# Performance work log

Measured on AMD Instinct MI355X. Metric: run time of the kernel, lower is better.

The kernel has to match this reference:

```python
import jax, jax.numpy as jnp
import numpy as np

N_NODES = 100000


def _add_self_loops(edge_index, n):
    loop = jnp.arange(n, dtype=edge_index.dtype)
    src = jnp.concatenate([edge_index[0], loop])
    dst = jnp.concatenate([edge_index[1], loop])
    return src, dst


def _gcn_conv(x, src, dst, dinv_src, dinv_dst, W, b, n):
    # linear transform first (PyG GCNConv), then normalized scatter-add
    h = x @ W                                   # [N, out]
    msg = h[src] * (dinv_src * dinv_dst)[:, None]  # [E+N, out] gather
    out = jax.ops.segment_sum(msg, dst, num_segments=n)
    return out + b


def reference(x, edge_index, W0, b0, W1, b1, Wf, bf):
    n = N_NODES
    src, dst = _add_self_loops(edge_index, n)
    ones = jnp.ones(src.shape[0], dtype=x.dtype)
    deg = jax.ops.segment_sum(ones, dst, num_segments=n)
    dinv = jnp.where(deg > 0, jax.lax.rsqrt(jnp.maximum(deg, 1.0)), 0.0)
    dinv_src = dinv[src]
    dinv_dst = dinv[dst]

    h = jax.nn.relu(_gcn_conv(x, src, dst, dinv_src, dinv_dst, W0, b0, n))
    h = jax.nn.relu(_gcn_conv(h, src, dst, dinv_src, dinv_dst, W1, b1, n))
    return h @ Wf + bf


def setup_inputs() -> dict:
    key = jax.random.key(0)
    ks = jax.random.split(key, 8)
    n, e, f, h = N_NODES, 1600000, 32, 32
    return {
        "x": jax.random.normal(ks[0], (n, f), dtype=jnp.float32),
        "edge_index": jax.random.randint(ks[1], (2, e), 0, n, dtype=jnp.int64),
        "W0": jax.random.normal(ks[2], (f, h), dtype=jnp.float32) / np.sqrt(f),
        "b0": jnp.zeros((h,), dtype=jnp.float32),
        "W1": jax.random.normal(ks[3], (h, h), dtype=jnp.float32) / np.sqrt(h),
        "b1": jnp.zeros((h,), dtype=jnp.float32),
        "Wf": jax.random.normal(ks[4], (h, h), dtype=jnp.float32) / np.sqrt(h),
        "bf": jnp.zeros((h,), dtype=jnp.float32),
    }
```

## Files before the change

### kernel.cpp

```cpp
#include <hip/hip_runtime.h>
#include <hip/hip_fp16.h>


#define GNN_F 32
#define NBKT 391
#define BCAP 5120
#define CHUNK 8192

__global__ __launch_bounds__(256) void k_fused1(
    const float* __restrict__ x, const float* __restrict__ W0,
    __half* __restrict__ t,
    const int* __restrict__ src, const int* __restrict__ dst,
    int* bcnt, int* __restrict__ queue,
    int n, int e, int gemmBlocks) {
    __shared__ float Wl[32 * 32];
    __shared__ int hist4[4 * NBKT], curs[NBKT], base[NBKT];
    int tid = threadIdx.x;

    if (blockIdx.x < gemmBlocks) {
        if (blockIdx.x == 0 && tid < 4) {
            uint4 z = make_uint4(0u, 0u, 0u, 0u);
            ((uint4*)(t + (size_t)n * 32))[tid] = z;
        }
        ((float4*)Wl)[tid] = ((const float4*)W0)[tid];
        __syncthreads();
        int r = blockIdx.x * 256 + tid;
        if (r >= n) return;
        float xr[32];
        const float4* in4 = (const float4*)(x + (size_t)r * 32);
#pragma unroll
        for (int j = 0; j < 8; ++j) {
            float4 v = in4[j];
            xr[4 * j + 0] = v.x; xr[4 * j + 1] = v.y;
            xr[4 * j + 2] = v.z; xr[4 * j + 3] = v.w;
        }
        float acc[32];
#pragma unroll
        for (int c = 0; c < 32; ++c) acc[c] = 0.0f;
#pragma unroll
        for (int k = 0; k < 32; ++k) {
            float xv = xr[k];
#pragma unroll
            for (int c = 0; c < 32; ++c) acc[c] = fmaf(xv, Wl[k * 32 + c], acc[c]);
        }
        uint4* tp = (uint4*)(t + (size_t)r * 32);
#pragma unroll
        for (int j = 0; j < 4; ++j) {
            __half2 h0 = __floats2half2_rn(acc[8 * j + 0], acc[8 * j + 1]);
            __half2 h1 = __floats2half2_rn(acc[8 * j + 2], acc[8 * j + 3]);
            __half2 h2 = __floats2half2_rn(acc[8 * j + 4], acc[8 * j + 5]);
            __half2 h3 = __floats2half2_rn(acc[8 * j + 6], acc[8 * j + 7]);
            uint4 o;
            o.x = *(unsigned*)&h0; o.y = *(unsigned*)&h1;
            o.z = *(unsigned*)&h2; o.w = *(unsigned*)&h3;
            tp[j] = o;
        }
    } else {
        int c0 = (blockIdx.x - gemmBlocks) * CHUNK;
        int g0 = c0 >> 2;
        int n4 = e >> 2;
        int cpy = (tid & 3) * NBKT;
        for (int i = tid; i < 4 * NBKT; i += 256) hist4[i] = 0;
        __syncthreads();
#pragma unroll
        for (int p = 0; p < CHUNK / 1024; ++p) {
            int g = g0 + p * 256 + tid;
            if (g < n4) {
                int4 d = ((const int4*)dst)[g];
                atomicAdd(&hist4[cpy + (((unsigned)d.x) >> 8)], 1);
                atomicAdd(&hist4[cpy + (((unsigned)d.y) >> 8)], 1);
                atomicAdd(&hist4[cpy + (((unsigned)d.z) >> 8)], 1);
                atomicAdd(&hist4[cpy + (((unsigned)d.w) >> 8)], 1);
            }
        }
        int tail0 = e & ~3;
        if (tail0 >= c0 && tail0 < c0 + CHUNK && tid < (e & 3))
            atomicAdd(&hist4[cpy + (((unsigned)dst[tail0 + tid]) >> 8)], 1);
        __syncthreads();
        for (int b = tid; b < NBKT; b += 256) {
            int h = hist4[b] + hist4[NBKT + b] + hist4[2 * NBKT + b] + hist4[3 * NBKT + b];
            base[b] = h ? atomicAdd(&bcnt[b], h) : 0;
            curs[b] = 0;
        }
        __syncthreads();
#pragma unroll
        for (int p = 0; p < CHUNK / 1024; ++p) {
            int g = g0 + p * 256 + tid;
            if (g < n4) {
                int4 d = ((const int4*)dst)[g];
                int4 sv = ((const int4*)src)[g];
                int b, l, slot;
                b = ((unsigned)d.x) >> 8; l = atomicAdd(&curs[b], 1); slot = base[b] + l;
                if (slot < BCAP) queue[(size_t)b * BCAP + slot] = (sv.x << 8) | (d.x & 255);
                b = ((unsigned)d.y) >> 8; l = atomicAdd(&curs[b], 1); slot = base[b] + l;
                if (slot < BCAP) queue[(size_t)b * BCAP + slot] = (sv.y << 8) | (d.y & 255);
                b = ((unsigned)d.z) >> 8; l = atomicAdd(&curs[b], 1); slot = base[b] + l;
                if (slot < BCAP) queue[(size_t)b * BCAP + slot] = (sv.z << 8) | (d.z & 255);
                b = ((unsigned)d.w) >> 8; l = atomicAdd(&curs[b], 1); slot = base[b] + l;
                if (slot < BCAP) queue[(size_t)b * BCAP + slot] = (sv.w << 8) | (d.w & 255);
            }
        }
        if (tail0 >= c0 && tail0 < c0 + CHUNK && tid < (e & 3)) {
            int j = tail0 + tid;
            int d = dst[j];
            int b = ((unsigned)d) >> 8;
            int l = atomicAdd(&curs[b], 1);
            int slot = base[b] + l;
            if (slot < BCAP) queue[(size_t)b * BCAP + slot] = (src[j] << 8) | (d & 255);
        }
    }
}

__global__ __launch_bounds__(256) void k_build(
    const int* __restrict__ bcnt, const int* __restrict__ queue,
    int* __restrict__ csr, int* __restrict__ rs, float* __restrict__ dinv,
    __half* __restrict__ t, int n) {
    __shared__ int red[256];
    __shared__ int hist2[2 * 256], sh[256], cur[256];
    __shared__ float dsh[256];
    int b = blockIdx.x;
    int tid = threadIdx.x;

    int part = 0;
    for (int i = tid; i < b; i += 256) {
        int v = bcnt[i];
        part += (v > BCAP ? BCAP : v);
    }
    red[tid] = part;
    hist2[tid] = 0;
    hist2[256 + tid] = 0;
    __syncthreads();
#pragma unroll
    for (int off = 128; off > 0; off >>= 1) {
        if (tid < off) red[tid] += red[tid + off];
        __syncthreads();
    }
    int bbase = red[0];

    int len = bcnt[b];
    if (len > BCAP) len = BCAP;
    const int* q = queue + (size_t)b * BCAP;

    int cpy = (tid & 1) << 8;
    for (int i = tid; i < len; i += 256) atomicAdd(&hist2[cpy + (q[i] & 255)], 1);
    __syncthreads();
    int c = hist2[tid] + hist2[256 + tid];
    sh[tid] = c;
    __syncthreads();
    for (int off = 1; off < 256; off <<= 1) {
        int xv = (tid >= off) ? sh[tid - off] : 0;
        __syncthreads();
        sh[tid] += xv;
        __syncthreads();
    }
    int myStart = bbase + sh[tid] - c;
    int node = (b << 8) + tid;
    float dv = rsqrtf((float)(c + 1));
    if (node < n) {
        rs[node] = myStart;
        dinv[node] = dv;
    }
    if (b == (int)gridDim.x - 1 && tid == 255) rs[n] = myStart + c;
    dsh[tid] = dv;
    cur[tid] = myStart;
    __syncthreads();
    for (int i = tid; i < len; i += 256) {
        int qq = q[i];
        int p = atomicAdd(&cur[qq & 255], 1);
        csr[p] = ((unsigned)qq) >> 8;
    }
    int rows = n - (b << 8);
    if (rows > 256) rows = 256;
    if (rows < 0) rows = 0;
    uint4* t4 = (uint4*)(t + ((size_t)b << 8) * 32);
    for (int i = tid; i < rows * 4; i += 256) {
        float d = dsh[i >> 2];
        uint4 v = t4[i];
        __half2 h0 = *(__half2*)&v.x, h1 = *(__half2*)&v.y;
        __half2 h2 = *(__half2*)&v.z, h3 = *(__half2*)&v.w;
        float2 f0 = __half22float2(h0), f1 = __half22float2(h1);
        float2 f2 = __half22float2(h2), f3 = __half22float2(h3);
        h0 = __floats2half2_rn(f0.x * d, f0.y * d);
        h1 = __floats2half2_rn(f1.x * d, f1.y * d);
        h2 = __floats2half2_rn(f2.x * d, f2.y * d);
        h3 = __floats2half2_rn(f3.x * d, f3.y * d);
        v.x = *(unsigned*)&h0; v.y = *(unsigned*)&h1;
        v.z = *(unsigned*)&h2; v.w = *(unsigned*)&h3;
        t4[i] = v;
    }
}

#define LOAD4(u, A, B)                                         \
    {                                                          \
        uint2 raw = ((const uint2*)(t + (size_t)(u) * 32))[j]; \
        __half2 p0 = *(__half2*)&raw.x;                        \
        __half2 p1 = *(__half2*)&raw.y;                        \
        A = __half22float2(p0);                                \
        B = __half22float2(p1);                                \
    }

#define GIDX(k_, uvar)                       \
    {                                        \
        int ik = e + (k_);                   \
        bool ok = ik < e1;                   \
        uvar = csr[ok ? ik : last];          \
        uvar = ok ? uvar : n;                \
    }

#define GATHER_BODY()                                                          \
    int idx = blockIdx.x * 256 + threadIdx.x;                                  \
    int tid = threadIdx.x;                                                     \
    int row = idx >> 3;                                                        \
    bool live = row < n;                                                       \
    if (!live) row = n - 1;                                                    \
    int j = tid & 7;                                                           \
    int e0 = rs[row];                                                          \
    int e1 = rs[row + 1];                                                      \
    ((float4*)Wl)[tid] = ((const float4*)W)[tid];                              \
    __syncthreads();                                                           \
    int last = e1 - 1;                                                         \
    float2 sa, sb;                                                             \
    LOAD4(row, sa, sb);                                                        \
    float d = dinv[row];                                                       \
    float ax = 0.f, ay = 0.f, az = 0.f, aw = 0.f;                              \
    int e = e0;                                                                \
    int rem = e1 - e0;                                                         \
    int u0, u1, u2, u3, u4, u5, u6, u7;                                        \
    if (rem > 0) {                                                             \
        u0 = csr[e];                                                           \
        GIDX(1, u1) GIDX(2, u2) GIDX(3, u3)                                    \
        GIDX(4, u4) GIDX(5, u5) GIDX(6, u6) GIDX(7, u7)                        \
    }                                                                          \
    while (rem > 0) {                                                          \
        float2 a0, b0v, a1, b1v, a2, b2v, a3, b3v;                             \
        float2 a4, b4v, a5, b5v, a6, b6v, a7, b7v;                             \
        LOAD4(u0, a0, b0v); LOAD4(u1, a1, b1v);                                \
        LOAD4(u2, a2, b2v); LOAD4(u3, a3, b3v);                                \
        LOAD4(u4, a4, b4v); LOAD4(u5, a5, b5v);                                \
        LOAD4(u6, a6, b6v); LOAD4(u7, a7, b7v);                                \
        e += 8; rem -= 8;                                                      \
        if (rem > 0) {                                                         \
            u0 = csr[e];                                                       \
            GIDX(1, u1) GIDX(2, u2) GIDX(3, u3)                                \
            GIDX(4, u4) GIDX(5, u5) GIDX(6, u6) GIDX(7, u7)                    \
        }                                                                      \
        ax += ((a0.x + a1.x) + (a2.x + a3.x)) + ((a4.x + a5.x) + (a6.x + a7.x));\
        ay += ((a0.y + a1.y) + (a2.y + a3.y)) + ((a4.y + a5.y) + (a6.y + a7.y));\
        az += ((b0v.x + b1v.x) + (b2v.x + b3v.x)) + ((b4v.x + b5v.x) + (b6v.x + b7v.x));\
        aw += ((b0v.y + b1v.y) + (b2v.y + b3v.y)) + ((b4v.y + b5v.y) + (b6v.y + b7v.y));\
    }                                                                          \
    float4 pb4 = ((const float4*)preb)[j];                                     \
    float4 u4v;                                                                \
    u4v.x = fmaxf(d * (ax + sa.x) + pb4.x, 0.0f);                              \
    u4v.y = fmaxf(d * (ay + sa.y) + pb4.y, 0.0f);                              \
    u4v.z = fmaxf(d * (az + sb.x) + pb4.z, 0.0f);                              \
    u4v.w = fmaxf(d * (aw + sb.y) + pb4.w, 0.0f);                              \
    int wv = tid >> 6;                                                         \
    int g = (tid >> 3) & 7;                                                    \
    float* urow = ur + wv * 320 + g * 40;                                      \
    *(float4*)(urow + 4 * j) = u4v;                                            \
       \
                \
    asm volatile("s_waitcnt lgkmcnt(0)" ::: "memory");

__global__ __launch_bounds__(256) void k_gather_gemm(
    const int* __restrict__ rs, const int* __restrict__ csr,
    const float* __restrict__ dinv, const __half* __restrict__ t,
    const float* __restrict__ W, const float* __restrict__ preb,
    __half* __restrict__ t_out, int n) {
    __shared__ float Wl[32 * 32];
    __shared__ float ur[4 * 320];
    if (blockIdx.x == 0 && threadIdx.x < 4) {
        uint4 z = make_uint4(0u, 0u, 0u, 0u);
        ((uint4*)(t_out + (size_t)n * 32))[threadIdx.x] = z;
    }
    GATHER_BODY()
    float4 o = make_float4(0.f, 0.f, 0.f, 0.f);
#pragma unroll
    for (int k = 0; k < 32; ++k) {
        float uk = urow[k];
        float4 wv4 = ((const float4*)(Wl + k * 32))[j];
        o.x = fmaf(uk, wv4.x, o.x);
        o.y = fmaf(uk, wv4.y, o.y);
        o.z = fmaf(uk, wv4.z, o.z);
        o.w = fmaf(uk, wv4.w, o.w);
    }
    o.x *= d; o.y *= d; o.z *= d; o.w *= d;
    if (live) {
        __half2 h0 = __floats2half2_rn(o.x, o.y);
        __half2 h1 = __floats2half2_rn(o.z, o.w);
        uint2 pk;
        pk.x = *(unsigned*)&h0; pk.y = *(unsigned*)&h1;
        ((uint2*)(t_out + (size_t)row * 32))[j] = pk;
    }
}

__global__ __launch_bounds__(256) void k_gather_out(
    const int* __restrict__ rs, const int* __restrict__ csr,
    const float* __restrict__ dinv, const __half* __restrict__ t,
    const float* __restrict__ W, const float* __restrict__ preb,
    const float* __restrict__ postb, float* __restrict__ out, int n) {
    __shared__ float Wl[32 * 32];
    __shared__ float ur[4 * 320];
    GATHER_BODY()
    float4 o = ((const float4*)postb)[j];
#pragma unroll
    for (int k = 0; k < 32; ++k) {
        float uk = urow[k];
        float4 wv4 = ((const float4*)(Wl + k * 32))[j];
        o.x = fmaf(uk, wv4.x, o.x);
        o.y = fmaf(uk, wv4.y, o.y);
        o.z = fmaf(uk, wv4.z, o.z);
        o.w = fmaf(uk, wv4.w, o.w);
    }
    if (live) ((float4*)(out + (size_t)row * 32))[j] = o;
}

extern "C" void kernel_launch(void* const* d_in, const int* in_sizes, int n_in,
                              void* d_out, int out_size, void* d_ws, size_t ws_size,
                              hipStream_t stream) {
    const float* x  = (const float*)d_in[0];
    const int*   ei = (const int*)d_in[1];
    const float* W0 = (const float*)d_in[2];
    const float* b0 = (const float*)d_in[3];
    const float* W1 = (const float*)d_in[4];
    const float* b1 = (const float*)d_in[5];
    const float* Wf = (const float*)d_in[6];
    const float* bf = (const float*)d_in[7];
    float* out = (float*)d_out;

    const int N = in_sizes[0] / GNN_F;
    const int E = in_sizes[1] / 2;
    const int* srcI = ei;
    const int* dstI = ei + E;

    const int gN = (N + 255) / 256;
    const int gG = (N * 8 + 255) / 256;
    const int nChunk = (E + CHUNK - 1) / CHUNK;

    char* ws = (char*)d_ws;
    size_t off = 0;
    auto alloc = [&](size_t bytes) {
        void* p = ws + off;
        off += (bytes + 127) & ~(size_t)127;
        return p;
    };
    int*    bcnt  = (int*)alloc((size_t)NBKT * 4);
    int*    rs    = (int*)alloc((size_t)(N + 1) * 4);
    float*  dinv  = (float*)alloc((size_t)N * 4);
    int*    queue = (int*)alloc((size_t)NBKT * BCAP * 4);
    int*    csr   = (int*)alloc((size_t)E * 4);
    __half* t_a   = (__half*)alloc((size_t)(N + 1) * GNN_F * 2);
    __half* t_b   = (__half*)alloc((size_t)(N + 1) * GNN_F * 2);
    (void)ws_size;

    hipMemsetAsync(bcnt, 0, (size_t)NBKT * 4, stream);

    k_fused1<<<gN + nChunk, 256, 0, stream>>>(x, W0, t_a, srcI, dstI, bcnt,
                                              queue, N, E, gN);
    k_build<<<NBKT, 256, 0, stream>>>(bcnt, queue, csr, rs, dinv, t_a, N);

    k_gather_gemm<<<gG, 256, 0, stream>>>(rs, csr, dinv, t_a, W1, b0, t_b, N);

    k_gather_out<<<gG, 256, 0, stream>>>(rs, csr, dinv, t_b, Wf, b1, bf, out, N);
}
```

Before: 162.6 us.

## Software-pipeline neighbor feature loads and use shuffles for per-row GEMM

The gather loop now issues the next batch of eight neighbor feature loads before reducing the current batch, a software pipeline that keeps more memory requests in flight per thread. The small per-row 32x32 GEMM also drops its shared-memory staging buffer: each thread's activation values are broadcast within the 8-lane row group via __shfl instead of being written to and read from LDS. This saves LDS traffic and shared memory but raises register pressure from the doubled load buffers, which could lower occupancy.

```diff
diff --git a/kernel.cpp b/kernel.cpp
--- a/kernel.cpp
+++ b/kernel.cpp
@@ -225,43 +225,63 @@
     float ax = 0.f, ay = 0.f, az = 0.f, aw = 0.f;                              \
     int e = e0;                                                                \
     int rem = e1 - e0;                                                         \
-    int u0, u1, u2, u3, u4, u5, u6, u7;                                        \
-    if (rem > 0) {                                                             \
+    float2 a0, b0v, a1, b1v, a2, b2v, a3, b3v;                                 \
+    float2 a4, b4v, a5, b5v, a6, b6v, a7, b7v;                                 \
+    if (rem > 0) {             \
+        int u0, u1, u2, u3, u4, u5, u6, u7;                                    \
         u0 = csr[e];                                                           \
         GIDX(1, u1) GIDX(2, u2) GIDX(3, u3)                                    \
         GIDX(4, u4) GIDX(5, u5) GIDX(6, u6) GIDX(7, u7)                        \
-    }                                                                          \
-    while (rem > 0) {                                                          \
-        float2 a0, b0v, a1, b1v, a2, b2v, a3, b3v;                             \
-        float2 a4, b4v, a5, b5v, a6, b6v, a7, b7v;                             \
         LOAD4(u0, a0, b0v); LOAD4(u1, a1, b1v);                                \
         LOAD4(u2, a2, b2v); LOAD4(u3, a3, b3v);                                \
         LOAD4(u4, a4, b4v); LOAD4(u5, a5, b5v);                                \
         LOAD4(u6, a6, b6v); LOAD4(u7, a7, b7v);                                \
+    }                                                                          \
+    while (rem > 0) {                                                          \
         e += 8; rem -= 8;                                                      \
-        if (rem > 0) {                                                         \
-            u0 = csr[e];                                                       \
-            GIDX(1, u1) GIDX(2, u2) GIDX(3, u3)                                \
-            GIDX(4, u4) GIDX(5, u5) GIDX(6, u6) GIDX(7, u7)                    \
+        float2 na0, nb0, na1, nb1, na2, nb2, na3, nb3;                         \
+        float2 na4, nb4, na5, nb5, na6, nb6, na7, nb7;                         \
+        if (rem > 0) {     \
+            int v0, v1, v2, v3, v4, v5, v6, v7;                                \
+            v0 = csr[e];                                                       \
+            GIDX(1, v1) GIDX(2, v2) GIDX(3, v3)                                \
+            GIDX(4, v4) GIDX(5, v5) GIDX(6, v6) GIDX(7, v7)                    \
+            LOAD4(v0, na0, nb0); LOAD4(v1, na1, nb1);                          \
+            LOAD4(v2, na2, nb2); LOAD4(v3, na3, nb3);                          \
+            LOAD4(v4, na4, nb4); LOAD4(v5, na5, nb5);                          \
+            LOAD4(v6, na6, nb6); LOAD4(v7, na7, nb7);                          \
         }                                                                      \
         ax += ((a0.x + a1.x) + (a2.x + a3.x)) + ((a4.x + a5.x) + (a6.x + a7.x));\
         ay += ((a0.y + a1.y) + (a2.y + a3.y)) + ((a4.y + a5.y) + (a6.y + a7.y));\
         az += ((b0v.x + b1v.x) + (b2v.x + b3v.x)) + ((b4v.x + b5v.x) + (b6v.x + b7v.x));\
         aw += ((b0v.y + b1v.y) + (b2v.y + b3v.y)) + ((b4v.y + b5v.y) + (b6v.y + b7v.y));\
+        if (rem > 0) {                                                         \
+            a0 = na0; b0v = nb0; a1 = na1; b1v = nb1;                          \
+            a2 = na2; b2v = nb2; a3 = na3; b3v = nb3;                          \
+            a4 = na4; b4v = nb4; a5 = na5; b5v = nb5;                          \
+            a6 = na6; b6v = nb6; a7 = na7; b7v = nb7;                          \
+        }                                                                      \
     }                                                                          \
     float4 pb4 = ((const float4*)preb)[j];                                     \
     float4 u4v;                                                                \
     u4v.x = fmaxf(d * (ax + sa.x) + pb4.x, 0.0f);                              \
     u4v.y = fmaxf(d * (ay + sa.y) + pb4.y, 0.0f);                              \
     u4v.z = fmaxf(d * (az + sb.x) + pb4.z, 0.0f);                              \
-    u4v.w = fmaxf(d * (aw + sb.y) + pb4.w, 0.0f);                              \
-    int wv = tid >> 6;                                                         \
-    int g = (tid >> 3) & 7;                                                    \
-    float* urow = ur + wv * 320 + g * 40;                                      \
-    *(float4*)(urow + 4 * j) = u4v;                                            \
-       \
-                \
-    asm volatile("s_waitcnt lgkmcnt(0)" ::: "memory");
+    u4v.w = fmaxf(d * (aw + sb.y) + pb4.w, 0.0f);
+
+#define GEMM_FMA(o_)                                                           \
+    _Pragma("unroll")                                                          \
+    for (int k = 0; k < 32; ++k) {                                             \
+        float comp = ((k & 3) == 0) ? u4v.x                                    \
+                   : ((k & 3) == 1) ? u4v.y                                    \
+                   : ((k & 3) == 2) ? u4v.z : u4v.w;                           \
+        float uk = __shfl(comp, k >> 2, 8);                                    \
+        float4 wv4 = ((const float4*)(Wl + k * 32))[j];                        \
+        o_.x = fmaf(uk, wv4.x, o_.x);                                          \
+        o_.y = fmaf(uk, wv4.y, o_.y);                                          \
+        o_.z = fmaf(uk, wv4.z, o_.z);                                          \
+        o_.w = fmaf(uk, wv4.w, o_.w);                                          \
+    }
 
 __global__ __launch_bounds__(256) void k_gather_gemm(
     const int* __restrict__ rs, const int* __restrict__ csr,
@@ -269,22 +289,13 @@
     const float* __restrict__ W, const float* __restrict__ preb,
     __half* __restrict__ t_out, int n) {
     __shared__ float Wl[32 * 32];
-    __shared__ float ur[4 * 320];
     if (blockIdx.x == 0 && threadIdx.x < 4) {
         uint4 z = make_uint4(0u, 0u, 0u, 0u);
         ((uint4*)(t_out + (size_t)n * 32))[threadIdx.x] = z;
     }
     GATHER_BODY()
     float4 o = make_float4(0.f, 0.f, 0.f, 0.f);
-#pragma unroll
-    for (int k = 0; k < 32; ++k) {
-        float uk = urow[k];
-        float4 wv4 = ((const float4*)(Wl + k * 32))[j];
-        o.x = fmaf(uk, wv4.x, o.x);
-        o.y = fmaf(uk, wv4.y, o.y);
-        o.z = fmaf(uk, wv4.z, o.z);
-        o.w = fmaf(uk, wv4.w, o.w);
-    }
+    GEMM_FMA(o)
     o.x *= d; o.y *= d; o.z *= d; o.w *= d;
     if (live) {
         __half2 h0 = __floats2half2_rn(o.x, o.y);
@@ -301,18 +312,9 @@
     const float* __restrict__ W, const float* __restrict__ preb,
     const float* __restrict__ postb, float* __restrict__ out, int n) {
     __shared__ float Wl[32 * 32];
-    __shared__ float ur[4 * 320];
     GATHER_BODY()
     float4 o = ((const float4*)postb)[j];
-#pragma unroll
-    for (int k = 0; k < 32; ++k) {
-        float uk = urow[k];
-        float4 wv4 = ((const float4*)(Wl + k * 32))[j];
-        o.x = fmaf(uk, wv4.x, o.x);
-        o.y = fmaf(uk, wv4.y, o.y);
-        o.z = fmaf(uk, wv4.z, o.z);
-        o.w = fmaf(uk, wv4.w, o.w);
-    }
+    GEMM_FMA(o)
     if (live) ((float4*)(out + (size_t)row * 32))[j] = o;
 }
 
```

Measured after the change: 178.1 us. 9.5% more time.

## Build CSR via global per-node degree atomics and scatter instead of bucket queue

Applied to the files above, without the earlier changes.

Replaces the two-level bucketed queue CSR build with a per-node global degree count (global atomics in the histogram pass), a prefix-scan in k_build, and a separate k_scatter kernel that places each source into the CSR using global atomic cursors. This removes the intermediate queue buffer, its write and re-read, and the BCAP overflow truncation. In exchange it adds 1.6M global atomics for degree counting and another 1.6M for scattering, with random-address CSR writes and an extra kernel launch. Within-row neighbor order becomes nondeterministic.

```diff
diff --git a/kernel.cpp b/kernel.cpp
--- a/kernel.cpp
+++ b/kernel.cpp
@@ -4,17 +4,16 @@
 
 #define GNN_F 32
 #define NBKT 391
-#define BCAP 5120
 #define CHUNK 8192
 
 __global__ __launch_bounds__(256) void k_fused1(
     const float* __restrict__ x, const float* __restrict__ W0,
     __half* __restrict__ t,
-    const int* __restrict__ src, const int* __restrict__ dst,
-    int* bcnt, int* __restrict__ queue,
+    const int* __restrict__ dst,
+    int* __restrict__ bcnt, int* __restrict__ deg,
     int n, int e, int gemmBlocks) {
     __shared__ float Wl[32 * 32];
-    __shared__ int hist4[4 * NBKT], curs[NBKT], base[NBKT];
+    __shared__ int hist4[4 * NBKT];
     int tid = threadIdx.x;
 
     if (blockIdx.x < gemmBlocks) {
@@ -71,64 +70,39 @@
                 atomicAdd(&hist4[cpy + (((unsigned)d.y) >> 8)], 1);
                 atomicAdd(&hist4[cpy + (((unsigned)d.z) >> 8)], 1);
                 atomicAdd(&hist4[cpy + (((unsigned)d.w) >> 8)], 1);
+                atomicAdd(&deg[d.x], 1);
+                atomicAdd(&deg[d.y], 1);
+                atomicAdd(&deg[d.z], 1);
+                atomicAdd(&deg[d.w], 1);
             }
         }
         int tail0 = e & ~3;
-        if (tail0 >= c0 && tail0 < c0 + CHUNK && tid < (e & 3))
-            atomicAdd(&hist4[cpy + (((unsigned)dst[tail0 + tid]) >> 8)], 1);
+        if (tail0 >= c0 && tail0 < c0 + CHUNK && tid < (e & 3)) {
+            int d = dst[tail0 + tid];
+            atomicAdd(&hist4[cpy + (((unsigned)d) >> 8)], 1);
+            atomicAdd(&deg[d], 1);
+        }
         __syncthreads();
         for (int b = tid; b < NBKT; b += 256) {
             int h = hist4[b] + hist4[NBKT + b] + hist4[2 * NBKT + b] + hist4[3 * NBKT + b];
-            base[b] = h ? atomicAdd(&bcnt[b], h) : 0;
-            curs[b] = 0;
-        }
-        __syncthreads();
-#pragma unroll
-        for (int p = 0; p < CHUNK / 1024; ++p) {
-            int g = g0 + p * 256 + tid;
-            if (g < n4) {
-                int4 d = ((const int4*)dst)[g];
-                int4 sv = ((const int4*)src)[g];
-                int b, l, slot;
-                b = ((unsigned)d.x) >> 8; l = atomicAdd(&curs[b], 1); slot = base[b] + l;
-                if (slot < BCAP) queue[(size_t)b * BCAP + slot] = (sv.x << 8) | (d.x & 255);
-                b = ((unsigned)d.y) >> 8; l = atomicAdd(&curs[b], 1); slot = base[b] + l;
-                if (slot < BCAP) queue[(size_t)b * BCAP + slot] = (sv.y << 8) | (d.y & 255);
-                b = ((unsigned)d.z) >> 8; l = atomicAdd(&curs[b], 1); slot = base[b] + l;
-                if (slot < BCAP) queue[(size_t)b * BCAP + slot] = (sv.z << 8) | (d.z & 255);
-                b = ((unsigned)d.w) >> 8; l = atomicAdd(&curs[b], 1); slot = base[b] + l;
-                if (slot < BCAP) queue[(size_t)b * BCAP + slot] = (sv.w << 8) | (d.w & 255);
-            }
-        }
-        if (tail0 >= c0 && tail0 < c0 + CHUNK && tid < (e & 3)) {
-            int j = tail0 + tid;
-            int d = dst[j];
-            int b = ((unsigned)d) >> 8;
-            int l = atomicAdd(&curs[b], 1);
-            int slot = base[b] + l;
-            if (slot < BCAP) queue[(size_t)b * BCAP + slot] = (src[j] << 8) | (d & 255);
+            if (h) atomicAdd(&bcnt[b], h);
         }
     }
 }
 
 __global__ __launch_bounds__(256) void k_build(
-    const int* __restrict__ bcnt, const int* __restrict__ queue,
-    int* __restrict__ csr, int* __restrict__ rs, float* __restrict__ dinv,
+    const int* __restrict__ bcnt, const int* __restrict__ deg,
+    int* __restrict__ rs, int* __restrict__ cur, float* __restrict__ dinv,
     __half* __restrict__ t, int n) {
     __shared__ int red[256];
-    __shared__ int hist2[2 * 256], sh[256], cur[256];
+    __shared__ int sh[256];
     __shared__ float dsh[256];
     int b = blockIdx.x;
     int tid = threadIdx.x;
 
     int part = 0;
-    for (int i = tid; i < b; i += 256) {
-        int v = bcnt[i];
-        part += (v > BCAP ? BCAP : v);
-    }
+    for (int i = tid; i < b; i += 256) part += bcnt[i];
     red[tid] = part;
-    hist2[tid] = 0;
-    hist2[256 + tid] = 0;
     __syncthreads();
 #pragma unroll
     for (int off = 128; off > 0; off >>= 1) {
@@ -137,14 +111,8 @@
     }
     int bbase = red[0];
 
-    int len = bcnt[b];
-    if (len > BCAP) len = BCAP;
-    const int* q = queue + (size_t)b * BCAP;
-
-    int cpy = (tid & 1) << 8;
-    for (int i = tid; i < len; i += 256) atomicAdd(&hist2[cpy + (q[i] & 255)], 1);
-    __syncthreads();
-    int c = hist2[tid] + hist2[256 + tid];
+    int node = (b << 8) + tid;
+    int c = (node < n) ? deg[node] : 0;
     sh[tid] = c;
     __syncthreads();
     for (int off = 1; off < 256; off <<= 1) {
@@ -154,21 +122,15 @@
         __syncthreads();
     }
     int myStart = bbase + sh[tid] - c;
-    int node = (b << 8) + tid;
     float dv = rsqrtf((float)(c + 1));
     if (node < n) {
         rs[node] = myStart;
         dinv[node] = dv;
+        cur[node] = myStart;
     }
     if (b == (int)gridDim.x - 1 && tid == 255) rs[n] = myStart + c;
     dsh[tid] = dv;
-    cur[tid] = myStart;
     __syncthreads();
-    for (int i = tid; i < len; i += 256) {
-        int qq = q[i];
-        int p = atomicAdd(&cur[qq & 255], 1);
-        csr[p] = ((unsigned)qq) >> 8;
-    }
     int rows = n - (b << 8);
     if (rows > 256) rows = 256;
     if (rows < 0) rows = 0;
@@ -187,6 +149,27 @@
         v.x = *(unsigned*)&h0; v.y = *(unsigned*)&h1;
         v.z = *(unsigned*)&h2; v.w = *(unsigned*)&h3;
         t4[i] = v;
+    }
+}
+
+__global__ __launch_bounds__(256) void k_scatter(
+    const int* __restrict__ src, const int* __restrict__ dst,
+    int* __restrict__ cur, int* __restrict__ csr, int e) {
+    int n4 = e >> 2;
+    int stride = gridDim.x * 256;
+    for (int g = blockIdx.x * 256 + threadIdx.x; g < n4; g += stride) {
+        int4 d = ((const int4*)dst)[g];
+        int4 s = ((const int4*)src)[g];
+        int p0 = atomicAdd(&cur[d.x], 1);
+        int p1 = atomicAdd(&cur[d.y], 1);
+        int p2 = atomicAdd(&cur[d.z], 1);
+        int p3 = atomicAdd(&cur[d.w], 1);
+        csr[p0] = s.x; csr[p1] = s.y; csr[p2] = s.z; csr[p3] = s.w;
+    }
+    if (blockIdx.x == 0 && threadIdx.x < (e & 3)) {
+        int j = (e & ~3) + threadIdx.x;
+        int p = atomicAdd(&cur[dst[j]], 1);
+        csr[p] = src[j];
     }
 }
 
@@ -346,19 +329,21 @@
         return p;
     };
     int*    bcnt  = (int*)alloc((size_t)NBKT * 4);
+    int*    deg   = (int*)alloc((size_t)N * 4);
     int*    rs    = (int*)alloc((size_t)(N + 1) * 4);
+    int*    cur   = (int*)alloc((size_t)N * 4);
     float*  dinv  = (float*)alloc((size_t)N * 4);
-    int*    queue = (int*)alloc((size_t)NBKT * BCAP * 4);
     int*    csr   = (int*)alloc((size_t)E * 4);
     __half* t_a   = (__half*)alloc((size_t)(N + 1) * GNN_F * 2);
     __half* t_b   = (__half*)alloc((size_t)(N + 1) * GNN_F * 2);
     (void)ws_size;
 
-    hipMemsetAsync(bcnt, 0, (size_t)NBKT * 4, stream);
-
-    k_fused1<<<gN + nChunk, 256, 0, stream>>>(x, W0, t_a, srcI, dstI, bcnt,
-                                              queue, N, E, gN);
-    k_build<<<NBKT, 256, 0, stream>>>(bcnt, queue, csr, rs, dinv, t_a, N);
+    hipMemsetAsync(bcnt, 0, (size_t)((char*)rs - (char*)bcnt), stream);
+
+    k_fused1<<<gN + nChunk, 256, 0, stream>>>(x, W0, t_a, dstI, bcnt, deg,
+                                              N, E, gN);
+    k_build<<<NBKT, 256, 0, stream>>>(bcnt, deg, rs, cur, dinv, t_a, N);
+    k_scatter<<<1024, 256, 0, stream>>>(srcI, dstI, cur, csr, E);
 
     k_gather_gemm<<<gG, 256, 0, stream>>>(rs, csr, dinv, t_a, W1, b0, t_b, N);
 
```

Measured after the change: 313.7 us. 92.9% more time.

## Halve bucket width to 128 rows and split feature prescale into its own kernel

Applied to the files above, without the earlier changes.

Bucket granularity drops from 256 to 128 destination rows, doubling the bucket count and halving per-bucket capacity, so k_build launches twice as many blocks, each doing less work. The dinv prescale of the transformed features moves out of k_build into a separate elementwise kernel. The goal is better occupancy and load balance in the CSR build. The cost is an extra kernel launch, larger shared histograms in k_fused1, and a tighter per-bucket capacity that raises the risk of overflow on skewed degree distributions.

```diff
diff --git a/kernel.cpp b/kernel.cpp
--- a/kernel.cpp
+++ b/kernel.cpp
@@ -3,8 +3,9 @@
 
 
 #define GNN_F 32
-#define NBKT 391
-#define BCAP 5120
+#define NBKT 782
+#define BROWS 128
+#define BCAP 2560
 #define CHUNK 8192
 
 __global__ __launch_bounds__(256) void k_fused1(
@@ -67,15 +68,15 @@
             int g = g0 + p * 256 + tid;
             if (g < n4) {
                 int4 d = ((const int4*)dst)[g];
-                atomicAdd(&hist4[cpy + (((unsigned)d.x) >> 8)], 1);
-                atomicAdd(&hist4[cpy + (((unsigned)d.y) >> 8)], 1);
-                atomicAdd(&hist4[cpy + (((unsigned)d.z) >> 8)], 1);
-                atomicAdd(&hist4[cpy + (((unsigned)d.w) >> 8)], 1);
+                atomicAdd(&hist4[cpy + (((unsigned)d.x) >> 7)], 1);
+                atomicAdd(&hist4[cpy + (((unsigned)d.y) >> 7)], 1);
+                atomicAdd(&hist4[cpy + (((unsigned)d.z) >> 7)], 1);
+                atomicAdd(&hist4[cpy + (((unsigned)d.w) >> 7)], 1);
             }
         }
         int tail0 = e & ~3;
         if (tail0 >= c0 && tail0 < c0 + CHUNK && tid < (e & 3))
-            atomicAdd(&hist4[cpy + (((unsigned)dst[tail0 + tid]) >> 8)], 1);
+            atomicAdd(&hist4[cpy + (((unsigned)dst[tail0 + tid]) >> 7)], 1);
         __syncthreads();
         for (int b = tid; b < NBKT; b += 256) {
             int h = hist4[b] + hist4[NBKT + b] + hist4[2 * NBKT + b] + hist4[3 * NBKT + b];
@@ -90,23 +91,23 @@
                 int4 d = ((const int4*)dst)[g];
                 int4 sv = ((const int4*)src)[g];
                 int b, l, slot;
-                b = ((unsigned)d.x) >> 8; l = atomicAdd(&curs[b], 1); slot = base[b] + l;
-                if (slot < BCAP) queue[(size_t)b * BCAP + slot] = (sv.x << 8) | (d.x & 255);
-                b = ((unsigned)d.y) >> 8; l = atomicAdd(&curs[b], 1); slot = base[b] + l;
-                if (slot < BCAP) queue[(size_t)b * BCAP + slot] = (sv.y << 8) | (d.y & 255);
-                b = ((unsigned)d.z) >> 8; l = atomicAdd(&curs[b], 1); slot = base[b] + l;
-                if (slot < BCAP) queue[(size_t)b * BCAP + slot] = (sv.z << 8) | (d.z & 255);
-                b = ((unsigned)d.w) >> 8; l = atomicAdd(&curs[b], 1); slot = base[b] + l;
-                if (slot < BCAP) queue[(size_t)b * BCAP + slot] = (sv.w << 8) | (d.w & 255);
+                b = ((unsigned)d.x) >> 7; l = atomicAdd(&curs[b], 1); slot = base[b] + l;
+                if (slot < BCAP) queue[(size_t)b * BCAP + slot] = (sv.x << 7) | (d.x & 127);
+                b = ((unsigned)d.y) >> 7; l = atomicAdd(&curs[b], 1); slot = base[b] + l;
+                if (slot < BCAP) queue[(size_t)b * BCAP + slot] = (sv.y << 7) | (d.y & 127);
+                b = ((unsigned)d.z) >> 7; l = atomicAdd(&curs[b], 1); slot = base[b] + l;
+                if (slot < BCAP) queue[(size_t)b * BCAP + slot] = (sv.z << 7) | (d.z & 127);
+                b = ((unsigned)d.w) >> 7; l = atomicAdd(&curs[b], 1); slot = base[b] + l;
+                if (slot < BCAP) queue[(size_t)b * BCAP + slot] = (sv.w << 7) | (d.w & 127);
             }
         }
         if (tail0 >= c0 && tail0 < c0 + CHUNK && tid < (e & 3)) {
-            int j = tail0 + tid;
-            int d = dst[j];
-            int b = ((unsigned)d) >> 8;
+            int jg = tail0 + tid;
+            int d = dst[jg];
+            int b = ((unsigned)d) >> 7;
             int l = atomicAdd(&curs[b], 1);
             int slot = base[b] + l;
-            if (slot < BCAP) queue[(size_t)b * BCAP + slot] = (src[j] << 8) | (d & 255);
+            if (slot < BCAP) queue[(size_t)b * BCAP + slot] = (src[jg] << 7) | (d & 127);
         }
     }
 }
@@ -114,10 +115,9 @@
 __global__ __launch_bounds__(256) void k_build(
     const int* __restrict__ bcnt, const int* __restrict__ queue,
     int* __restrict__ csr, int* __restrict__ rs, float* __restrict__ dinv,
-    __half* __restrict__ t, int n) {
+    int n) {
     __shared__ int red[256];
-    __shared__ int hist2[2 * 256], sh[256], cur[256];
-    __shared__ float dsh[256];
+    __shared__ int hist2[2 * BROWS], sh[BROWS], cur[BROWS];
     int b = blockIdx.x;
     int tid = threadIdx.x;
 
@@ -127,8 +127,7 @@
         part += (v > BCAP ? BCAP : v);
     }
     red[tid] = part;
-    hist2[tid] = 0;
-    hist2[256 + tid] = 0;
+    hist2[tid & 255] = 0;
     __syncthreads();
 #pragma unroll
     for (int off = 128; off > 0; off >>= 1) {
@@ -141,53 +140,57 @@
     if (len > BCAP) len = BCAP;
     const int* q = queue + (size_t)b * BCAP;
 
-    int cpy = (tid & 1) << 8;
-    for (int i = tid; i < len; i += 256) atomicAdd(&hist2[cpy + (q[i] & 255)], 1);
+    int cpy = (tid & 1) << 7;
+    for (int i = tid; i < len; i += 256) atomicAdd(&hist2[cpy + (q[i] & 127)], 1);
     __syncthreads();
-    int c = hist2[tid] + hist2[256 + tid];
-    sh[tid] = c;
+    int c = 0;
+    if (tid < BROWS) {
+        c = hist2[tid] + hist2[BROWS + tid];
+        sh[tid] = c;
+    }
     __syncthreads();
-    for (int off = 1; off < 256; off <<= 1) {
-        int xv = (tid >= off) ? sh[tid - off] : 0;
-        __syncthreads();
-        sh[tid] += xv;
-        __syncthreads();
-    }
-    int myStart = bbase + sh[tid] - c;
-    int node = (b << 8) + tid;
-    float dv = rsqrtf((float)(c + 1));
-    if (node < n) {
-        rs[node] = myStart;
-        dinv[node] = dv;
-    }
-    if (b == (int)gridDim.x - 1 && tid == 255) rs[n] = myStart + c;
-    dsh[tid] = dv;
-    cur[tid] = myStart;
+    for (int off = 1; off < BROWS; off <<= 1) {
+        int xv = (tid >= off && tid < BROWS) ? sh[tid - off] : 0;
+        __syncthreads();
+        if (tid < BROWS) sh[tid] += xv;
+        __syncthreads();
+    }
+    if (tid < BROWS) {
+        int myStart = bbase + sh[tid] - c;
+        int node = (b << 7) + tid;
+        if (node < n) {
+            rs[node] = myStart;
+            dinv[node] = rsqrtf((float)(c + 1));
+        }
+        if (b == (int)gridDim.x - 1 && tid == BROWS - 1) rs[n] = myStart + c;
+        cur[tid] = myStart;
+    }
     __syncthreads();
     for (int i = tid; i < len; i += 256) {
         int qq = q[i];
-        int p = atomicAdd(&cur[qq & 255], 1);
-        csr[p] = ((unsigned)qq) >> 8;
-    }
-    int rows = n - (b << 8);
-    if (rows > 256) rows = 256;
-    if (rows < 0) rows = 0;
-    uint4* t4 = (uint4*)(t + ((size_t)b << 8) * 32);
-    for (int i = tid; i < rows * 4; i += 256) {
-        float d = dsh[i >> 2];
-        uint4 v = t4[i];
-        __half2 h0 = *(__half2*)&v.x, h1 = *(__half2*)&v.y;
-        __half2 h2 = *(__half2*)&v.z, h3 = *(__half2*)&v.w;
-        float2 f0 = __half22float2(h0), f1 = __half22float2(h1);
-        float2 f2 = __half22float2(h2), f3 = __half22float2(h3);
-        h0 = __floats2half2_rn(f0.x * d, f0.y * d);
-        h1 = __floats2half2_rn(f1.x * d, f1.y * d);
-        h2 = __floats2half2_rn(f2.x * d, f2.y * d);
-        h3 = __floats2half2_rn(f3.x * d, f3.y * d);
-        v.x = *(unsigned*)&h0; v.y = *(unsigned*)&h1;
-        v.z = *(unsigned*)&h2; v.w = *(unsigned*)&h3;
-        t4[i] = v;
-    }
+        int p = atomicAdd(&cur[qq & 127], 1);
+        csr[p] = ((unsigned)qq) >> 7;
+    }
+}
+
+__global__ __launch_bounds__(256) void k_prescale(
+    const float* __restrict__ dinv, __half* __restrict__ t, int n) {
+    int i = blockIdx.x * 256 + threadIdx.x;
+    if (i >= n * 4) return;
+    float d = dinv[i >> 2];
+    uint4* t4 = (uint4*)t;
+    uint4 v = t4[i];
+    __half2 h0 = *(__half2*)&v.x, h1 = *(__half2*)&v.y;
+    __half2 h2 = *(__half2*)&v.z, h3 = *(__half2*)&v.w;
+    float2 f0 = __half22float2(h0), f1 = __half22float2(h1);
+    float2 f2 = __half22float2(h2), f3 = __half22float2(h3);
+    h0 = __floats2half2_rn(f0.x * d, f0.y * d);
+    h1 = __floats2half2_rn(f1.x * d, f1.y * d);
+    h2 = __floats2half2_rn(f2.x * d, f2.y * d);
+    h3 = __floats2half2_rn(f3.x * d, f3.y * d);
+    v.x = *(unsigned*)&h0; v.y = *(unsigned*)&h1;
+    v.z = *(unsigned*)&h2; v.w = *(unsigned*)&h3;
+    t4[i] = v;
 }
 
 #define LOAD4(u, A, B)                                         \
@@ -336,6 +339,7 @@
 
     const int gN = (N + 255) / 256;
     const int gG = (N * 8 + 255) / 256;
+    const int gP = (N * 4 + 255) / 256;
     const int nChunk = (E + CHUNK - 1) / CHUNK;
 
     char* ws = (char*)d_ws;
@@ -358,7 +362,8 @@
 
     k_fused1<<<gN + nChunk, 256, 0, stream>>>(x, W0, t_a, srcI, dstI, bcnt,
                                               queue, N, E, gN);
-    k_build<<<NBKT, 256, 0, stream>>>(bcnt, queue, csr, rs, dinv, t_a, N);
+    k_build<<<NBKT, 256, 0, stream>>>(bcnt, queue, csr, rs, dinv, N);
+    k_prescale<<<gP, 256, 0, stream>>>(dinv, t_a, N);
 
     k_gather_gemm<<<gG, 256, 0, stream>>>(rs, csr, dinv, t_a, W1, b0, t_b, N);
 
```

Result: no change. 164.9 us (+1.4%).
